# Performance work log

Measured on AMD Instinct MI355X. Metric: run time of the kernel, lower is better.

The kernel has to match this reference:

```python
import jax, jax.numpy as jnp
import numpy as np

N = 50000   # nodes
E = 800000  # edges (avg degree 16)
D = 64      # feature dim (in == out, so lin_self is Identity)
NEG_SLOPE = 0.2


def setup_inputs() -> dict:
    key = jax.random.key(0)
    ks = jax.random.split(key, 8)
    s = 1.0 / np.sqrt(D)
    return {
        "x": jax.random.normal(ks[0], (N, D), dtype=jnp.float32),
        "edge_index": jax.random.randint(ks[1], (2, E), 0, N, dtype=jnp.int64),
        "edge_attr": jax.random.uniform(ks[2], (E,), dtype=jnp.float32),
        "W_msg": jax.random.normal(ks[3], (D, D), dtype=jnp.float32) * s,
        "b_msg": jax.random.normal(ks[4], (D,), dtype=jnp.float32) * s,
        "W_edge": jax.random.normal(ks[5], (1, D), dtype=jnp.float32),
        "b_edge": jax.random.normal(ks[6], (D,), dtype=jnp.float32),
        "att": jax.random.normal(ks[7], (D,), dtype=jnp.float32) * s,
    }


def reference(x, edge_index, edge_attr, W_msg, b_msg, W_edge, b_edge, att):
    src, dst = edge_index[0], edge_index[1]
    # message: lin_msg(x_j) + lin_edge(edge_attr)           [E, D]
    msg = x[src] @ W_msg + b_msg + edge_attr[:, None] @ W_edge + b_edge
    # additive attention logits (heads=1)                   [E]
    logits = jnp.sum(jax.nn.leaky_relu(msg, NEG_SLOPE) * att, axis=-1)
    # segment softmax over destination nodes (PyG softmax, eps=1e-16)
    m = jax.ops.segment_max(logits, dst, num_segments=N)
    m = jnp.where(jnp.isneginf(m), 0.0, m)
    ex = jnp.exp(logits - m[dst])
    denom = jax.ops.segment_sum(ex, dst, num_segments=N)
    alpha = ex / (denom[dst] + 1e-16)
    weighted = msg * alpha[:, None]
    # scatter-max aggregation; empty segments -> 0 (PyG fill value)
    agg = jax.ops.segment_max(weighted, dst, num_segments=N)
    agg = jnp.where(jnp.isneginf(agg), 0.0, agg)
    # lin_self is Identity (in_channels == out_channels, skip_linear=False)
    return agg + x
```

## Files before the change

kernel.cpp:

```cpp
#include <hip/hip_runtime.h>

#define N_NODES 50000
#define N_EDGES 800000
#define DIM 64
#define NEG_SLOPE 0.2f
#define NEG_INF (-__builtin_inff())
#define NB      3125
#define MAXDEG  128

typedef _Float16 half8 __attribute__((ext_vector_type(8)));

__global__ __launch_bounds__(256) void k_pre(const float* __restrict__ x,
                                             const float* __restrict__ W,
                                             const float* __restrict__ b_msg,
                                             const float* __restrict__ b_edge,
                                             _Float16* __restrict__ xmh,
                                             const int* __restrict__ eidx,
                                             const float* __restrict__ eattr,
                                             unsigned* __restrict__ cnt,
                                             int2* __restrict__ elist) {
    __shared__ float Ws[DIM * DIM];
    __shared__ float xs[16 * DIM];
    int tid = threadIdx.x;
    int bid = blockIdx.x;

    int e = bid * 256 + tid;
    int    esrc = eidx[e];
    int    edst = eidx[N_EDGES + e];
    float  ea   = eattr[e];
    unsigned r  = atomicAdd(cnt + edst, 1u);

    const float4* W4 = (const float4*)W;
    float4* Ws4 = (float4*)Ws;
    #pragma unroll
    for (int i = 0; i < 4; ++i) Ws4[tid + 256 * i] = W4[tid + 256 * i];
    int base = bid * 16;
    ((float4*)xs)[tid] = ((const float4*)(x + (size_t)base * DIM))[tid];
    __syncthreads();

    if (r < MAXDEG)
        elist[((size_t)edst << 7) + r] = make_int2(esrc, __float_as_int(ea));

    int w = tid >> 6;
    int d = tid & 63;
    float bias = b_msg[d] + b_edge[d];
    float s0 = bias, s1 = bias, s2 = bias, s3 = bias;
    const float* xr = xs + (w * 4) * DIM;
    #pragma unroll
    for (int k = 0; k < DIM; ++k) {
        float wv = Ws[k * DIM + d];
        s0 = fmaf(xr[k], wv, s0);
        s1 = fmaf(xr[DIM + k], wv, s1);
        s2 = fmaf(xr[2 * DIM + k], wv, s2);
        s3 = fmaf(xr[3 * DIM + k], wv, s3);
    }
    _Float16* o = xmh + ((size_t)base + w * 4) * DIM + d;
    o[0] = (_Float16)s0;
    o[DIM] = (_Float16)s1;
    o[2 * DIM] = (_Float16)s2;
    o[3 * DIM] = (_Float16)s3;
}

__global__ __launch_bounds__(256) void k_aggregate(const half8* __restrict__ xm8,
                                                   const int2* __restrict__ elist,
                                                   const unsigned* __restrict__ cnt,
                                                   const float4* __restrict__ W_edge4,
                                                   const float4* __restrict__ att4,
                                                   const float4* __restrict__ x4,
                                                   float4* __restrict__ out4) {
    int node = blockIdx.x * 4 + (threadIdx.x >> 6);
    int lane = threadIdx.x & 63;
    int g = lane >> 3, t = lane & 7;
    unsigned deg = cnt[node];
    if (deg > MAXDEG) deg = MAXDEG;
    size_t obase = (size_t)node * 16 + 2 * t;
    if (deg == 0) {
        if (g == 0) { out4[obase] = x4[obase]; out4[obase + 1] = x4[obase + 1]; }
        return;
    }
    unsigned beg = (unsigned)node << 7;
    unsigned end = beg + deg;
    float4 wa = W_edge4[2 * t], wb = W_edge4[2 * t + 1];
    float4 aa = att4[2 * t],    ab = att4[2 * t + 1];
    float we[8] = {wa.x, wa.y, wa.z, wa.w, wb.x, wb.y, wb.z, wb.w};
    float at[8] = {aa.x, aa.y, aa.z, aa.w, ab.x, ab.y, ab.z, ab.w};

    unsigned idx = beg + (unsigned)g;
    bool act = idx < end;
    int2 e = elist[act ? idx : beg];
    half8 h = xm8[(size_t)e.x * 8 + t];

    float m = NEG_INF, denom = 0.f;
    float v[8];
    #pragma unroll
    for (int k = 0; k < 8; ++k) v[k] = 0.f;
    bool first = true;

    for (unsigned b = beg;; b += 8) {
        bool more = (b + 8) < end;
        int2 e2; half8 h2; bool a2 = false;
        if (more) {
            unsigned i2 = b + 8 + (unsigned)g;
            a2 = i2 < end;
            e2 = elist[a2 ? i2 : beg];
            h2 = xm8[(size_t)e2.x * 8 + t];
        }
        float ea = __int_as_float(e.y);
        float msg[8];
        float p = 0.f;
        #pragma unroll
        for (int k = 0; k < 8; ++k) {
            float f = (float)h[k];
            msg[k] = fmaf(ea, we[k], f);
            float lr = fmaxf(msg[k], NEG_SLOPE * msg[k]);
            p = fmaf(lr, at[k], p);
        }
        p += __shfl_xor(p, 1, 64);
        p += __shfl_xor(p, 2, 64);
        p += __shfl_xor(p, 4, 64);
        if (first) {
            if (act) {
                m = p; denom = 1.f;
                #pragma unroll
                for (int k = 0; k < 8; ++k) v[k] = msg[k];
            }
            first = false;
        } else if (act) {
            float M = fmaxf(m, p);
            float so = __expf(m - M);
            float sn = __expf(p - M);
            denom = fmaf(denom, so, sn);
            #pragma unroll
            for (int k = 0; k < 8; ++k)
                v[k] = fmaxf(v[k] * so, msg[k] * sn);
            m = M;
        }
        if (!more) break;
        e = e2; h = h2; act = a2;
    }
    bool has = denom > 0.f;
    float Ms = m;
    Ms = fmaxf(Ms, __shfl_xor(Ms, 8, 64));
    Ms = fmaxf(Ms, __shfl_xor(Ms, 16, 64));
    Ms = fmaxf(Ms, __shfl_xor(Ms, 32, 64));
    float s = has ? __expf(m - Ms) : 0.f;
    float dd = denom * s;
    dd += __shfl_xor(dd, 8, 64);
    dd += __shfl_xor(dd, 16, 64);
    dd += __shfl_xor(dd, 32, 64);
    float gv[8];
    #pragma unroll
    for (int k = 0; k < 8; ++k) {
        float gk = has ? v[k] * s : NEG_INF;
        gk = fmaxf(gk, __shfl_xor(gk, 8, 64));
        gk = fmaxf(gk, __shfl_xor(gk, 16, 64));
        gk = fmaxf(gk, __shfl_xor(gk, 32, 64));
        gv[k] = gk;
    }
    if (g == 0) {
        float inv = 1.0f / (dd + 1e-16f);
        float4 xa = x4[obase], xb = x4[obase + 1];
        float4 r0, r1;
        r0.x = fmaf(gv[0], inv, xa.x);
        r0.y = fmaf(gv[1], inv, xa.y);
        r0.z = fmaf(gv[2], inv, xa.z);
        r0.w = fmaf(gv[3], inv, xa.w);
        r1.x = fmaf(gv[4], inv, xb.x);
        r1.y = fmaf(gv[5], inv, xb.y);
        r1.z = fmaf(gv[6], inv, xb.z);
        r1.w = fmaf(gv[7], inv, xb.w);
        out4[obase] = r0;
        out4[obase + 1] = r1;
    }
}

extern "C" void kernel_launch(void* const* d_in, const int* in_sizes, int n_in,
                              void* d_out, int out_size, void* d_ws, size_t ws_size,
                              hipStream_t stream) {
    const float* x      = (const float*)d_in[0];
    const int*   eidx   = (const int*)d_in[1];
    const float* eattr  = (const float*)d_in[2];
    const float* W_msg  = (const float*)d_in[3];
    const float* b_msg  = (const float*)d_in[4];
    const float* W_edge = (const float*)d_in[5];
    const float* b_edge = (const float*)d_in[6];
    const float* att    = (const float*)d_in[7];
    float* out = (float*)d_out;

    _Float16* xmh   = (_Float16*)d_ws;
    int2*     elist = (int2*)(xmh + (size_t)N_NODES * DIM);
    unsigned* cnt   = (unsigned*)(elist + (size_t)N_NODES * MAXDEG);

    hipMemsetAsync(cnt, 0, (size_t)N_NODES * 4, stream);

    k_pre<<<NB, 256, 0, stream>>>(x, W_msg, b_msg, b_edge, xmh,
                                  eidx, eattr, cnt, elist);
    k_aggregate<<<N_NODES / 4, 256, 0, stream>>>(
        (const half8*)xmh, elist, cnt, (const float4*)W_edge,
        (const float4*)att, (const float4*)x, (float4*)out);
}
```

Before: 154.9 us.

## Map one 8-lane group per node in aggregation instead of one wavefront per node

```diff
diff --git a/kernel.cpp b/kernel.cpp
--- a/kernel.cpp
+++ b/kernel.cpp
@@ -68,41 +68,39 @@
                                                    const float4* __restrict__ att4,
                                                    const float4* __restrict__ x4,
                                                    float4* __restrict__ out4) {
-    int node = blockIdx.x * 4 + (threadIdx.x >> 6);
     int lane = threadIdx.x & 63;
+    int wv   = threadIdx.x >> 6;
     int g = lane >> 3, t = lane & 7;
+    int node = (blockIdx.x * 4 + wv) * 8 + g;
+    if (node >= N_NODES) return;
     unsigned deg = cnt[node];
     if (deg > MAXDEG) deg = MAXDEG;
     size_t obase = (size_t)node * 16 + 2 * t;
     if (deg == 0) {
-        if (g == 0) { out4[obase] = x4[obase]; out4[obase + 1] = x4[obase + 1]; }
+        out4[obase] = x4[obase];
+        out4[obase + 1] = x4[obase + 1];
         return;
     }
-    unsigned beg = (unsigned)node << 7;
-    unsigned end = beg + deg;
     float4 wa = W_edge4[2 * t], wb = W_edge4[2 * t + 1];
     float4 aa = att4[2 * t],    ab = att4[2 * t + 1];
     float we[8] = {wa.x, wa.y, wa.z, wa.w, wb.x, wb.y, wb.z, wb.w};
     float at[8] = {aa.x, aa.y, aa.z, aa.w, ab.x, ab.y, ab.z, ab.w};
 
-    unsigned idx = beg + (unsigned)g;
-    bool act = idx < end;
-    int2 e = elist[act ? idx : beg];
+    unsigned beg = (unsigned)node << 7;
+    int2  e = elist[beg];
     half8 h = xm8[(size_t)e.x * 8 + t];
 
     float m = NEG_INF, denom = 0.f;
     float v[8];
     #pragma unroll
     for (int k = 0; k < 8; ++k) v[k] = 0.f;
-    bool first = true;
 
-    for (unsigned b = beg;; b += 8) {
-        bool more = (b + 8) < end;
-        int2 e2; half8 h2; bool a2 = false;
+    unsigned i = 0;
+    while (true) {
+        bool more = (i + 1) < deg;
+        int2 e2; half8 h2;
         if (more) {
-            unsigned i2 = b + 8 + (unsigned)g;
-            a2 = i2 < end;
-            e2 = elist[a2 ? i2 : beg];
+            e2 = elist[beg + i + 1];
             h2 = xm8[(size_t)e2.x * 8 + t];
         }
         float ea = __int_as_float(e.y);
@@ -118,15 +116,12 @@
         p += __shfl_xor(p, 1, 64);
         p += __shfl_xor(p, 2, 64);
         p += __shfl_xor(p, 4, 64);
-        if (first) {
-            if (act) {
-                m = p; denom = 1.f;
-                #pragma unroll
-                for (int k = 0; k < 8; ++k) v[k] = msg[k];
-            }
-            first = false;
-        } else if (act) {
-            float M = fmaxf(m, p);
+        if (i == 0) {
+            m = p; denom = 1.f;
+            #pragma unroll
+            for (int k = 0; k < 8; ++k) v[k] = msg[k];
+        } else {
+            float M  = fmaxf(m, p);
             float so = __expf(m - M);
             float sn = __expf(p - M);
             denom = fmaf(denom, so, sn);
@@ -136,42 +131,21 @@
             m = M;
         }
         if (!more) break;
-        e = e2; h = h2; act = a2;
+        e = e2; h = h2; ++i;
     }
-    bool has = denom > 0.f;
-    float Ms = m;
-    Ms = fmaxf(Ms, __shfl_xor(Ms, 8, 64));
-    Ms = fmaxf(Ms, __shfl_xor(Ms, 16, 64));
-    Ms = fmaxf(Ms, __shfl_xor(Ms, 32, 64));
-    float s = has ? __expf(m - Ms) : 0.f;
-    float dd = denom * s;
-    dd += __shfl_xor(dd, 8, 64);
-    dd += __shfl_xor(dd, 16, 64);
-    dd += __shfl_xor(dd, 32, 64);
-    float gv[8];
-    #pragma unroll
-    for (int k = 0; k < 8; ++k) {
-        float gk = has ? v[k] * s : NEG_INF;
-        gk = fmaxf(gk, __shfl_xor(gk, 8, 64));
-        gk = fmaxf(gk, __shfl_xor(gk, 16, 64));
-        gk = fmaxf(gk, __shfl_xor(gk, 32, 64));
-        gv[k] = gk;
-    }
-    if (g == 0) {
-        float inv = 1.0f / (dd + 1e-16f);
-        float4 xa = x4[obase], xb = x4[obase + 1];
-        float4 r0, r1;
-        r0.x = fmaf(gv[0], inv, xa.x);
-        r0.y = fmaf(gv[1], inv, xa.y);
-        r0.z = fmaf(gv[2], inv, xa.z);
-        r0.w = fmaf(gv[3], inv, xa.w);
-        r1.x = fmaf(gv[4], inv, xb.x);
-        r1.y = fmaf(gv[5], inv, xb.y);
-        r1.z = fmaf(gv[6], inv, xb.z);
-        r1.w = fmaf(gv[7], inv, xb.w);
-        out4[obase] = r0;
-        out4[obase + 1] = r1;
-    }
+    float inv = 1.0f / (denom + 1e-16f);
+    float4 xa = x4[obase], xb = x4[obase + 1];
+    float4 r0, r1;
+    r0.x = fmaf(v[0], inv, xa.x);
+    r0.y = fmaf(v[1], inv, xa.y);
+    r0.z = fmaf(v[2], inv, xa.z);
+    r0.w = fmaf(v[3], inv, xa.w);
+    r1.x = fmaf(v[4], inv, xb.x);
+    r1.y = fmaf(v[5], inv, xb.y);
+    r1.z = fmaf(v[6], inv, xb.z);
+    r1.w = fmaf(v[7], inv, xb.w);
+    out4[obase] = r0;
+    out4[obase + 1] = r1;
 }
 
 extern "C" void kernel_launch(void* const* d_in, const int* in_sizes, int n_in,
@@ -195,7 +169,7 @@
 
     k_pre<<<NB, 256, 0, stream>>>(x, W_msg, b_msg, b_edge, xmh,
                                   eidx, eattr, cnt, elist);
-    k_aggregate<<<N_NODES / 4, 256, 0, stream>>>(
+    k_aggregate<<<(N_NODES + 31) / 32, 256, 0, stream>>>(
         (const half8*)xmh, elist, cnt, (const float4*)W_edge,
         (const float4*)att, (const float4*)x, (float4*)out);
 }
```

New measurement: 154.4 us. Within noise of the previous version (-0.3%).
